# Performance work log

Hardware: AMD Instinct MI355X
Metric: run time of the kernel (lower is better)

Reference implementation:

```python
import jax, jax.numpy as jnp
import numpy as np

N = 16384
DIM_IN = 128
DIM_OUT = 128
HIDDEN = (DIM_IN + DIM_OUT) // 2  # 128


def setup_inputs() -> dict:
    key = jax.random.key(0)
    ks = jax.random.split(key, 8)
    s_in = 1.0 / np.sqrt(DIM_IN)
    s_h = 1.0 / np.sqrt(HIDDEN)
    return {
        "x": jax.random.normal(ks[0], (N, DIM_IN), dtype=jnp.float32),
        "adj": jax.random.uniform(ks[1], (N, N), dtype=jnp.float32) * (1.0 / N),
        "W2": jax.random.uniform(ks[2], (DIM_IN, HIDDEN), minval=-s_in, maxval=s_in, dtype=jnp.float32),
        "b2": jnp.zeros((HIDDEN,), dtype=jnp.float32),
        "W4": jax.random.uniform(ks[3], (HIDDEN, DIM_OUT), minval=-s_h, maxval=s_h, dtype=jnp.float32),
        "b4": jnp.zeros((DIM_OUT,), dtype=jnp.float32),
        "res_w": jax.random.uniform(ks[4], (DIM_OUT, HIDDEN), minval=-s_h, maxval=s_h, dtype=jnp.float32),
        "res_b": jax.random.uniform(ks[5], (DIM_OUT,), minval=-s_h, maxval=s_h, dtype=jnp.float32),
    }


def gcn(x, adj, W, b):
    # GraphConvolution: support = x @ W; out = adj @ support + b
    return adj @ (x @ W) + b


def reference(x, adj, W2, b2, W4, b4, res_w, res_b):
    local_hidden = gcn(x, adj, W2, b2)          # [N, HIDDEN]
    local_cross = gcn(local_hidden, adj, W4, b4)  # [N, DIM_OUT]
    # addRes: residual linear projection of local_hidden
    embed = local_cross + local_hidden @ res_w.T + res_b
    return embed
```

## Files before the change

kernel.cpp:

```cpp
#include <hip/hip_runtime.h>
#include <hip/hip_bf16.h>

#define MN 16384
#define SPLITS 4
#define KSLICE (MN / SPLITS)
#define BK 64
#define NSTEPS (KSLICE / BK)

typedef float f32x4 __attribute__((ext_vector_type(4)));
typedef int   i32x4 __attribute__((ext_vector_type(4)));

#define A8S 32768.0f
#define SB1 64.0f
#define SB2 4096.0f
#define SC1 (1.0f / (32768.0f * 64.0f))
#define SC2 (1.0f / (32768.0f * 4096.0f))

__device__ __forceinline__ void async16(void* lds, const void* g) {
  __builtin_amdgcn_global_load_lds(
      (const __attribute__((address_space(1))) unsigned int*)g,
      (__attribute__((address_space(3))) unsigned int*)lds, 16, 0, 0);
}


__global__ __launch_bounds__(256)
void k1_xw2(const float* __restrict__ x, const float* __restrict__ W2,
            unsigned char* __restrict__ B1) {
  __shared__ __align__(16) float xs[64 * 128];
  const int t = threadIdx.x;
  const long rowbase = (long)blockIdx.x * 64;
  const f32x4* xg = (const f32x4*)(x + rowbase * 128);
  f32x4* xl = (f32x4*)xs;
#pragma unroll
  for (int i = 0; i < 8; ++i) xl[t + 256 * i] = xg[t + 256 * i];
  __syncthreads();
  const int r0 = (t >> 5) * 8;
  const int c0 = (t & 31) * 4;
  float acc[8][4] = {};
  for (int k = 0; k < 128; k += 4) {
    f32x4 w[4];
#pragma unroll
    for (int kk = 0; kk < 4; ++kk) w[kk] = *(const f32x4*)(W2 + (k + kk) * 128 + c0);
#pragma unroll
    for (int i = 0; i < 8; ++i) {
      f32x4 xv = *(const f32x4*)(xs + (r0 + i) * 128 + k);
#pragma unroll
      for (int kk = 0; kk < 4; ++kk)
#pragma unroll
        for (int j = 0; j < 4; ++j) acc[i][j] += xv[kk] * w[kk][j];
    }
  }
  const long U = (rowbase + r0) >> 3;
  i32x4 wv0, wv1;
#pragma unroll
  for (int j = 0; j < 4; ++j) {
    int lo = __builtin_amdgcn_cvt_pk_fp8_f32(acc[0][j] * SB1, acc[1][j] * SB1, 0, false);
    lo     = __builtin_amdgcn_cvt_pk_fp8_f32(acc[2][j] * SB1, acc[3][j] * SB1, lo, true);
    int hi = __builtin_amdgcn_cvt_pk_fp8_f32(acc[4][j] * SB1, acc[5][j] * SB1, 0, false);
    hi     = __builtin_amdgcn_cvt_pk_fp8_f32(acc[6][j] * SB1, acc[7][j] * SB1, hi, true);
    if (j < 2) { wv0[2 * j] = lo; wv0[2 * j + 1] = hi; }
    else       { wv1[2 * (j - 2)] = lo; wv1[2 * (j - 2) + 1] = hi; }
  }
  *(i32x4*)(B1 + (U * 128 + c0) * 8)      = wv0;
  *(i32x4*)(B1 + (U * 128 + c0) * 8 + 16) = wv1;
}

template <int AMODE>
__global__ __launch_bounds__(256, 4)
void big_mm(const float* __restrict__ A, const unsigned char* __restrict__ A8r,
            unsigned char* __restrict__ A8w, const unsigned char* __restrict__ B8,
            float sc, float* __restrict__ P) {
  __shared__ __align__(16) unsigned char Bs[3 * 8192];
  const int tid  = threadIdx.x;
  const int wid  = tid >> 6;
  const int lane = tid & 63;
  const int g    = lane >> 4;
  const int cl   = lane & 15;
  const int tile_m = blockIdx.x & 255;
  const int s      = blockIdx.x >> 8;
  const long k0 = (long)s * KSLICE;

  const char* bsrc = (const char*)B8 + k0 * 128 + (long)tid * 16;
  const float* aptr = nullptr;
  if constexpr (AMODE != 1)
    aptr = A + (long)(tile_m * 64 + wid * 16 + cl) * MN + k0 + 16 * g;
  const long c8base = (long)blockIdx.x * (64L * 4096) + (long)tid * 16;

  f32x4 acc[8] = {};

  {
    unsigned char* d0 = Bs + wid * 1024;
    async16(d0, bsrc);          async16(d0 + 4096, bsrc + 4096);
    unsigned char* d1 = Bs + 8192 + wid * 1024;
    async16(d1, bsrc + 8192);   async16(d1 + 4096, bsrc + 12288);
  }
  f32x4 a0n, a1n, a2n, a3n;
  i32x4 q8n;
  if constexpr (AMODE == 1) {
    q8n = *(const i32x4*)(A8r + c8base);
  } else {
    a0n = *(const f32x4*)aptr;       a1n = *(const f32x4*)(aptr + 4);
    a2n = *(const f32x4*)(aptr + 8); a3n = *(const f32x4*)(aptr + 12);
  }
  __syncthreads();

  int cur = 0, nxt = 2;
  for (int t = 0; t < NSTEPS; ++t) {
    if (t + 2 < NSTEPS) {
      unsigned char* d = Bs + nxt * 8192 + wid * 1024;
      const char* src = bsrc + (long)(t + 2) * 8192;
      async16(d, src);  async16(d + 4096, src + 4096);
    }
    __builtin_amdgcn_sched_barrier(0);

    i32x4 pk;
    if constexpr (AMODE == 1) {
      pk = q8n;
      if (t + 1 < NSTEPS)
        q8n = *(const i32x4*)(A8r + c8base + (long)(t + 1) * 4096);
    } else {
      f32x4 a0 = a0n, a1 = a1n, a2 = a2n, a3 = a3n;
      if (t + 1 < NSTEPS) {
        const float* ap = aptr + (long)(t + 1) * BK;
        a0n = *(const f32x4*)ap;       a1n = *(const f32x4*)(ap + 4);
        a2n = *(const f32x4*)(ap + 8); a3n = *(const f32x4*)(ap + 12);
      }
      pk[0] = __builtin_amdgcn_cvt_pk_fp8_f32(a0[0] * A8S, a0[1] * A8S, 0, false);
      pk[0] = __builtin_amdgcn_cvt_pk_fp8_f32(a0[2] * A8S, a0[3] * A8S, pk[0], true);
      pk[1] = __builtin_amdgcn_cvt_pk_fp8_f32(a1[0] * A8S, a1[1] * A8S, 0, false);
      pk[1] = __builtin_amdgcn_cvt_pk_fp8_f32(a1[2] * A8S, a1[3] * A8S, pk[1], true);
      pk[2] = __builtin_amdgcn_cvt_pk_fp8_f32(a2[0] * A8S, a2[1] * A8S, 0, false);
      pk[2] = __builtin_amdgcn_cvt_pk_fp8_f32(a2[2] * A8S, a2[3] * A8S, pk[2], true);
      pk[3] = __builtin_amdgcn_cvt_pk_fp8_f32(a3[0] * A8S, a3[1] * A8S, 0, false);
      pk[3] = __builtin_amdgcn_cvt_pk_fp8_f32(a3[2] * A8S, a3[3] * A8S, pk[3], true);
      if constexpr (AMODE == 0)
        __builtin_nontemporal_store(pk, (i32x4*)(A8w + c8base + (long)t * 4096));
    }
    const long alo = ((long)(unsigned)pk[1] << 32) | (unsigned)pk[0];
    const long ahi = ((long)(unsigned)pk[3] << 32) | (unsigned)pk[2];

    const char* bb = (const char*)Bs + cur * 8192 + g * 2048 + cl * 8;
#pragma unroll
    for (int c = 0; c < 8; ++c) {
      long b0 = *(const long*)(bb + c * 128);
      long b1 = *(const long*)(bb + 1024 + c * 128);
      acc[c] = __builtin_amdgcn_mfma_f32_16x16x32_fp8_fp8(alo, b0, acc[c], 0, 0, 0);
      acc[c] = __builtin_amdgcn_mfma_f32_16x16x32_fp8_fp8(ahi, b1, acc[c], 0, 0, 0);
    }

    if (t < NSTEPS - 2) {
      if constexpr (AMODE == 0)      asm volatile("s_waitcnt vmcnt(7)" ::: "memory");
      else if constexpr (AMODE == 2) asm volatile("s_waitcnt vmcnt(6)" ::: "memory");
      else                           asm volatile("s_waitcnt vmcnt(3)" ::: "memory");
    } else {
      asm volatile("s_waitcnt vmcnt(0)" ::: "memory");
    }
    __builtin_amdgcn_s_barrier();
    cur = (cur == 2) ? 0 : cur + 1;
    nxt = (nxt == 2) ? 0 : nxt + 1;
  }

  float* pb = P + ((long)s * MN + tile_m * 64 + wid * 16) * 128;
#pragma unroll
  for (int c = 0; c < 8; ++c)
#pragma unroll
    for (int q = 0; q < 4; ++q)
      __builtin_nontemporal_store(acc[c][q] * sc,
                                  &pb[(g * 4 + q) * 128 + 16 * c + cl]);
}

__global__ __launch_bounds__(256)
void k3_mid(const float* __restrict__ P, const float* __restrict__ b2,
            const float* __restrict__ W4, const float* __restrict__ res_w,
            const float* __restrict__ b4, const float* __restrict__ res_b,
            unsigned char* __restrict__ B2, float* __restrict__ Rr) {
  __shared__ __align__(16) float hs[64 * 128];
  const int t = threadIdx.x;
  const long rowbase = (long)blockIdx.x * 64;
  const long base = rowbase * 32;
  const f32x4* P0 = (const f32x4*)P + base;
  const f32x4* P1 = (const f32x4*)P + (long)MN * 32 + base;
  const f32x4* P2 = (const f32x4*)P + 2L * MN * 32 + base;
  const f32x4* P3 = (const f32x4*)P + 3L * MN * 32 + base;
  const f32x4* b2v = (const f32x4*)b2;
  f32x4* hl = (f32x4*)hs;
#pragma unroll
  for (int i = 0; i < 8; ++i) {
    int idx = t + 256 * i;
    f32x4 v = __builtin_nontemporal_load(P0 + idx);
    v += __builtin_nontemporal_load(P1 + idx);
    v += __builtin_nontemporal_load(P2 + idx);
    v += __builtin_nontemporal_load(P3 + idx);
    hl[idx] = v + b2v[idx & 31];
  }
  __syncthreads();
  const int r0 = (t >> 5) * 8;
  const int c0 = (t & 31) * 4;
  float acc2[8][4] = {};
  float accR[8][4] = {};
  for (int k = 0; k < 128; k += 4) {
    f32x4 w4v[4], rwv[4];
#pragma unroll
    for (int kk = 0; kk < 4; ++kk) w4v[kk] = *(const f32x4*)(W4 + (k + kk) * 128 + c0);
#pragma unroll
    for (int j = 0; j < 4; ++j) rwv[j] = *(const f32x4*)(res_w + (c0 + j) * 128 + k);
#pragma unroll
    for (int i = 0; i < 8; ++i) {
      f32x4 xv = *(const f32x4*)(hs + (r0 + i) * 128 + k);
#pragma unroll
      for (int kk = 0; kk < 4; ++kk)
#pragma unroll
        for (int j = 0; j < 4; ++j) {
          acc2[i][j] += xv[kk] * w4v[kk][j];
          accR[i][j] += xv[kk] * rwv[j][kk];
        }
    }
  }
  const long U = (rowbase + r0) >> 3;
  i32x4 wv0, wv1;
#pragma unroll
  for (int j = 0; j < 4; ++j) {
    int lo = __builtin_amdgcn_cvt_pk_fp8_f32(acc2[0][j] * SB2, acc2[1][j] * SB2, 0, false);
    lo     = __builtin_amdgcn_cvt_pk_fp8_f32(acc2[2][j] * SB2, acc2[3][j] * SB2, lo, true);
    int hi = __builtin_amdgcn_cvt_pk_fp8_f32(acc2[4][j] * SB2, acc2[5][j] * SB2, 0, false);
    hi     = __builtin_amdgcn_cvt_pk_fp8_f32(acc2[6][j] * SB2, acc2[7][j] * SB2, hi, true);
    if (j < 2) { wv0[2 * j] = lo; wv0[2 * j + 1] = hi; }
    else       { wv1[2 * (j - 2)] = lo; wv1[2 * (j - 2) + 1] = hi; }
  }
  *(i32x4*)(B2 + (U * 128 + c0) * 8)      = wv0;
  *(i32x4*)(B2 + (U * 128 + c0) * 8 + 16) = wv1;

  const f32x4 b4v = *(const f32x4*)(b4 + c0);
  const f32x4 rbv = *(const f32x4*)(res_b + c0);
#pragma unroll
  for (int i = 0; i < 8; ++i) {
    f32x4 rv;
#pragma unroll
    for (int j = 0; j < 4; ++j) rv[j] = accR[i][j];
    rv += b4v + rbv;
    *(f32x4*)(Rr + (rowbase + r0 + i) * 128 + c0) = rv;
  }
}

__global__ __launch_bounds__(256)
void k5_out(const float* __restrict__ P, const float* __restrict__ Rr,
            float* __restrict__ out) {
  const long i = (long)blockIdx.x * 256 + threadIdx.x;
  const f32x4* P0 = (const f32x4*)P;
  const f32x4* P1 = P0 + (long)MN * 32;
  const f32x4* P2 = P0 + 2L * MN * 32;
  const f32x4* P3 = P0 + 3L * MN * 32;
  f32x4 v = __builtin_nontemporal_load(P0 + i);
  v += __builtin_nontemporal_load(P1 + i);
  v += __builtin_nontemporal_load(P2 + i);
  v += __builtin_nontemporal_load(P3 + i);
  v += *((const f32x4*)Rr + i);
  __builtin_nontemporal_store(v, (f32x4*)out + i);
}

extern "C" void kernel_launch(void* const* d_in, const int* in_sizes, int n_in,
                              void* d_out, int out_size, void* d_ws, size_t ws_size,
                              hipStream_t stream) {
  const float* x     = (const float*)d_in[0];
  const float* adj   = (const float*)d_in[1];
  const float* W2    = (const float*)d_in[2];
  const float* b2    = (const float*)d_in[3];
  const float* W4    = (const float*)d_in[4];
  const float* b4    = (const float*)d_in[5];
  const float* res_w = (const float*)d_in[6];
  const float* res_b = (const float*)d_in[7];
  float* out = (float*)d_out;

  char* ws = (char*)d_ws;
  unsigned char* B1 = (unsigned char*)ws;
  unsigned char* B2 = (unsigned char*)(ws + (4L << 20));
  float* Rr = (float*)(ws + (8L << 20));
  float* P  = (float*)(ws + (16L << 20));
  unsigned char* A8 = (unsigned char*)(ws + (48L << 20));

  const size_t need = (48L << 20) + (size_t)MN * MN;
  const bool fp8_copy = ws_size >= need;

  k1_xw2<<<dim3(256), dim3(256), 0, stream>>>(x, W2, B1);
  if (fp8_copy) {
    big_mm<0><<<dim3(256 * SPLITS), dim3(256), 0, stream>>>(adj, nullptr, A8, B1, SC1, P);
    k3_mid<<<dim3(256), dim3(256), 0, stream>>>(P, b2, W4, res_w, b4, res_b, B2, Rr);
    big_mm<1><<<dim3(256 * SPLITS), dim3(256), 0, stream>>>(nullptr, A8, nullptr, B2, SC2, P);
  } else {
    big_mm<2><<<dim3(256 * SPLITS), dim3(256), 0, stream>>>(adj, nullptr, nullptr, B1, SC1, P);
    k3_mid<<<dim3(256), dim3(256), 0, stream>>>(P, b2, W4, res_w, b4, res_b, B2, Rr);
    big_mm<2><<<dim3(256 * SPLITS), dim3(256), 0, stream>>>(adj, nullptr, nullptr, B2, SC2, P);
  }
  k5_out<<<dim3(2048), dim3(256), 0, stream>>>(P, Rr, out);
}
```

Measured before the change: 443.5 us.

## Double K-step and rows per block, switch to double-buffered B staging

```diff
diff --git a/kernel.cpp b/kernel.cpp
--- a/kernel.cpp
+++ b/kernel.cpp
@@ -4,7 +4,7 @@
 #define MN 16384
 #define SPLITS 4
 #define KSLICE (MN / SPLITS)
-#define BK 64
+#define BK 128
 #define NSTEPS (KSLICE / BK)
 
 typedef float f32x4 __attribute__((ext_vector_type(4)));
@@ -66,101 +66,97 @@
 }
 
 template <int AMODE>
-__global__ __launch_bounds__(256, 4)
+__global__ __launch_bounds__(512, 4)
 void big_mm(const float* __restrict__ A, const unsigned char* __restrict__ A8r,
             unsigned char* __restrict__ A8w, const unsigned char* __restrict__ B8,
             float sc, float* __restrict__ P) {
-  __shared__ __align__(16) unsigned char Bs[3 * 8192];
+  __shared__ __align__(16) unsigned char Bs[2][16384];
   const int tid  = threadIdx.x;
   const int wid  = tid >> 6;
   const int lane = tid & 63;
   const int g    = lane >> 4;
   const int cl   = lane & 15;
-  const int tile_m = blockIdx.x & 255;
-  const int s      = blockIdx.x >> 8;
+  const int tile_m = blockIdx.x & 127;
+  const int s      = blockIdx.x >> 7;
   const long k0 = (long)s * KSLICE;
 
   const char* bsrc = (const char*)B8 + k0 * 128 + (long)tid * 16;
   const float* aptr = nullptr;
   if constexpr (AMODE != 1)
-    aptr = A + (long)(tile_m * 64 + wid * 16 + cl) * MN + k0 + 16 * g;
-  const long c8base = (long)blockIdx.x * (64L * 4096) + (long)tid * 16;
+    aptr = A + (long)(tile_m * 128 + wid * 16 + cl) * MN + k0 + 32 * g;
+  const long c8base = (long)blockIdx.x * (NSTEPS * 16384L) + (long)tid * 32;
 
   f32x4 acc[8] = {};
 
   {
-    unsigned char* d0 = Bs + wid * 1024;
-    async16(d0, bsrc);          async16(d0 + 4096, bsrc + 4096);
-    unsigned char* d1 = Bs + 8192 + wid * 1024;
-    async16(d1, bsrc + 8192);   async16(d1 + 4096, bsrc + 12288);
-  }
-  f32x4 a0n, a1n, a2n, a3n;
-  i32x4 q8n;
+    unsigned char* d = &Bs[0][0] + wid * 1024;
+    async16(d, bsrc);
+    async16(d + 8192, bsrc + 8192);
+  }
+  i32x4 av0, av1;
   if constexpr (AMODE == 1) {
-    q8n = *(const i32x4*)(A8r + c8base);
-  } else {
-    a0n = *(const f32x4*)aptr;       a1n = *(const f32x4*)(aptr + 4);
-    a2n = *(const f32x4*)(aptr + 8); a3n = *(const f32x4*)(aptr + 12);
+    av0 = *(const i32x4*)(A8r + c8base);
+    av1 = *(const i32x4*)(A8r + c8base + 16);
   }
   __syncthreads();
 
-  int cur = 0, nxt = 2;
-  for (int t = 0; t < NSTEPS; ++t) {
-    if (t + 2 < NSTEPS) {
-      unsigned char* d = Bs + nxt * 8192 + wid * 1024;
-      const char* src = bsrc + (long)(t + 2) * 8192;
-      async16(d, src);  async16(d + 4096, src + 4096);
+  for (int T = 0; T < NSTEPS; ++T) {
+    if (T + 1 < NSTEPS) {
+      unsigned char* d = &Bs[(T + 1) & 1][0] + wid * 1024;
+      const char* src = bsrc + (long)(T + 1) * 16384;
+      async16(d, src);
+      async16(d + 8192, src + 8192);
     }
     __builtin_amdgcn_sched_barrier(0);
 
-    i32x4 pk;
+    int pk[8];
+    i32x4 nav0, nav1;
     if constexpr (AMODE == 1) {
-      pk = q8n;
-      if (t + 1 < NSTEPS)
-        q8n = *(const i32x4*)(A8r + c8base + (long)(t + 1) * 4096);
+      if (T + 1 < NSTEPS) {
+        const unsigned char* ap = A8r + c8base + (long)(T + 1) * 16384;
+        nav0 = *(const i32x4*)ap;
+        nav1 = *(const i32x4*)(ap + 16);
+      }
+      pk[0] = av0[0]; pk[1] = av0[1]; pk[2] = av0[2]; pk[3] = av0[3];
+      pk[4] = av1[0]; pk[5] = av1[1]; pk[6] = av1[2]; pk[7] = av1[3];
     } else {
-      f32x4 a0 = a0n, a1 = a1n, a2 = a2n, a3 = a3n;
-      if (t + 1 < NSTEPS) {
-        const float* ap = aptr + (long)(t + 1) * BK;
-        a0n = *(const f32x4*)ap;       a1n = *(const f32x4*)(ap + 4);
-        a2n = *(const f32x4*)(ap + 8); a3n = *(const f32x4*)(ap + 12);
-      }
-      pk[0] = __builtin_amdgcn_cvt_pk_fp8_f32(a0[0] * A8S, a0[1] * A8S, 0, false);
-      pk[0] = __builtin_amdgcn_cvt_pk_fp8_f32(a0[2] * A8S, a0[3] * A8S, pk[0], true);
-      pk[1] = __builtin_amdgcn_cvt_pk_fp8_f32(a1[0] * A8S, a1[1] * A8S, 0, false);
-      pk[1] = __builtin_amdgcn_cvt_pk_fp8_f32(a1[2] * A8S, a1[3] * A8S, pk[1], true);
-      pk[2] = __builtin_amdgcn_cvt_pk_fp8_f32(a2[0] * A8S, a2[1] * A8S, 0, false);
-      pk[2] = __builtin_amdgcn_cvt_pk_fp8_f32(a2[2] * A8S, a2[3] * A8S, pk[2], true);
-      pk[3] = __builtin_amdgcn_cvt_pk_fp8_f32(a3[0] * A8S, a3[1] * A8S, 0, false);
-      pk[3] = __builtin_amdgcn_cvt_pk_fp8_f32(a3[2] * A8S, a3[3] * A8S, pk[3], true);
-      if constexpr (AMODE == 0)
-        __builtin_nontemporal_store(pk, (i32x4*)(A8w + c8base + (long)t * 4096));
-    }
-    const long alo = ((long)(unsigned)pk[1] << 32) | (unsigned)pk[0];
-    const long ahi = ((long)(unsigned)pk[3] << 32) | (unsigned)pk[2];
-
-    const char* bb = (const char*)Bs + cur * 8192 + g * 2048 + cl * 8;
-#pragma unroll
-    for (int c = 0; c < 8; ++c) {
-      long b0 = *(const long*)(bb + c * 128);
-      long b1 = *(const long*)(bb + 1024 + c * 128);
-      acc[c] = __builtin_amdgcn_mfma_f32_16x16x32_fp8_fp8(alo, b0, acc[c], 0, 0, 0);
-      acc[c] = __builtin_amdgcn_mfma_f32_16x16x32_fp8_fp8(ahi, b1, acc[c], 0, 0, 0);
-    }
-
-    if (t < NSTEPS - 2) {
-      if constexpr (AMODE == 0)      asm volatile("s_waitcnt vmcnt(7)" ::: "memory");
-      else if constexpr (AMODE == 2) asm volatile("s_waitcnt vmcnt(6)" ::: "memory");
-      else                           asm volatile("s_waitcnt vmcnt(3)" ::: "memory");
-    } else {
-      asm volatile("s_waitcnt vmcnt(0)" ::: "memory");
+      const float* ap = aptr + (long)T * BK;
+      f32x4 av[8];
+#pragma unroll
+      for (int i = 0; i < 8; ++i) av[i] = *(const f32x4*)(ap + 4 * i);
+#pragma unroll
+      for (int d = 0; d < 8; ++d) {
+        int w = __builtin_amdgcn_cvt_pk_fp8_f32(av[d][0] * A8S, av[d][1] * A8S, 0, false);
+        pk[d] = __builtin_amdgcn_cvt_pk_fp8_f32(av[d][2] * A8S, av[d][3] * A8S, w, true);
+      }
+      if constexpr (AMODE == 0) {
+        i32x4 s1 = {pk[0], pk[1], pk[2], pk[3]};
+        i32x4 s2 = {pk[4], pk[5], pk[6], pk[7]};
+        unsigned char* wp = A8w + c8base + (long)T * 16384;
+        __builtin_nontemporal_store(s1, (i32x4*)wp);
+        __builtin_nontemporal_store(s2, (i32x4*)(wp + 16));
+      }
+    }
+
+    const char* bb = (const char*)&Bs[T & 1][0] + g * 4096 + cl * 8;
+#pragma unroll
+    for (int j = 0; j < 4; ++j) {
+      const long a = ((long)(unsigned)pk[2 * j + 1] << 32) | (unsigned)pk[2 * j];
+#pragma unroll
+      for (int c = 0; c < 8; ++c) {
+        long b = *(const long*)(bb + j * 1024 + c * 128);
+        acc[c] = __builtin_amdgcn_mfma_f32_16x16x32_fp8_fp8(a, b, acc[c], 0, 0, 0);
+      }
+    }
+
+    if constexpr (AMODE == 1) {
+      if (T + 1 < NSTEPS) asm volatile("s_waitcnt vmcnt(2)" ::: "memory");
+      av0 = nav0; av1 = nav1;
     }
     __builtin_amdgcn_s_barrier();
-    cur = (cur == 2) ? 0 : cur + 1;
-    nxt = (nxt == 2) ? 0 : nxt + 1;
-  }
-
-  float* pb = P + ((long)s * MN + tile_m * 64 + wid * 16) * 128;
+  }
+
+  float* pb = P + ((long)s * MN + tile_m * 128 + wid * 16) * 128;
 #pragma unroll
   for (int c = 0; c < 8; ++c)
 #pragma unroll
@@ -283,13 +279,13 @@
 
   k1_xw2<<<dim3(256), dim3(256), 0, stream>>>(x, W2, B1);
   if (fp8_copy) {
-    big_mm<0><<<dim3(256 * SPLITS), dim3(256), 0, stream>>>(adj, nullptr, A8, B1, SC1, P);
+    big_mm<0><<<dim3(128 * SPLITS), dim3(512), 0, stream>>>(adj, nullptr, A8, B1, SC1, P);
     k3_mid<<<dim3(256), dim3(256), 0, stream>>>(P, b2, W4, res_w, b4, res_b, B2, Rr);
-    big_mm<1><<<dim3(256 * SPLITS), dim3(256), 0, stream>>>(nullptr, A8, nullptr, B2, SC2, P);
+    big_mm<1><<<dim3(128 * SPLITS), dim3(512), 0, stream>>>(nullptr, A8, nullptr, B2, SC2, P);
   } else {
-    big_mm<2><<<dim3(256 * SPLITS), dim3(256), 0, stream>>>(adj, nullptr, nullptr, B1, SC1, P);
+    big_mm<2><<<dim3(128 * SPLITS), dim3(512), 0, stream>>>(adj, nullptr, nullptr, B1, SC1, P);
     k3_mid<<<dim3(256), dim3(256), 0, stream>>>(P, b2, W4, res_w, b4, res_b, B2, Rr);
-    big_mm<2><<<dim3(256 * SPLITS), dim3(256), 0, stream>>>(adj, nullptr, nullptr, B2, SC2, P);
+    big_mm<2><<<dim3(128 * SPLITS), dim3(512), 0, stream>>>(adj, nullptr, nullptr, B2, SC2, P);
   }
   k5_out<<<dim3(2048), dim3(256), 0, stream>>>(P, Rr, out);
 }
```

New measurement: 595.0 us. 34.2% more time.

## Double-buffer B tiles in two-step supersteps to halve barriers in big_mm

Applied to the files above, without the earlier changes.

```diff
diff --git a/kernel.cpp b/kernel.cpp
--- a/kernel.cpp
+++ b/kernel.cpp
@@ -6,6 +6,7 @@
 #define KSLICE (MN / SPLITS)
 #define BK 64
 #define NSTEPS (KSLICE / BK)
+#define NSUPER (NSTEPS / 2)
 
 typedef float f32x4 __attribute__((ext_vector_type(4)));
 typedef int   i32x4 __attribute__((ext_vector_type(4)));
@@ -70,7 +71,7 @@
 void big_mm(const float* __restrict__ A, const unsigned char* __restrict__ A8r,
             unsigned char* __restrict__ A8w, const unsigned char* __restrict__ B8,
             float sc, float* __restrict__ P) {
-  __shared__ __align__(16) unsigned char Bs[3 * 8192];
+  __shared__ __align__(16) unsigned char Bs[2][16384];
   const int tid  = threadIdx.x;
   const int wid  = tid >> 6;
   const int lane = tid & 63;
@@ -89,10 +90,9 @@
   f32x4 acc[8] = {};
 
   {
-    unsigned char* d0 = Bs + wid * 1024;
-    async16(d0, bsrc);          async16(d0 + 4096, bsrc + 4096);
-    unsigned char* d1 = Bs + 8192 + wid * 1024;
-    async16(d1, bsrc + 8192);   async16(d1 + 4096, bsrc + 12288);
+    unsigned char* d = &Bs[0][0] + wid * 1024;
+    async16(d, bsrc);                 async16(d + 4096, bsrc + 4096);
+    async16(d + 8192, bsrc + 8192);   async16(d + 12288, bsrc + 12288);
   }
   f32x4 a0n, a1n, a2n, a3n;
   i32x4 q8n;
@@ -104,60 +104,63 @@
   }
   __syncthreads();
 
-  int cur = 0, nxt = 2;
-  for (int t = 0; t < NSTEPS; ++t) {
-    if (t + 2 < NSTEPS) {
-      unsigned char* d = Bs + nxt * 8192 + wid * 1024;
-      const char* src = bsrc + (long)(t + 2) * 8192;
-      async16(d, src);  async16(d + 4096, src + 4096);
+  for (int m = 0; m < NSUPER; ++m) {
+    if (m + 1 < NSUPER) {
+      unsigned char* d = &Bs[(m + 1) & 1][0] + wid * 1024;
+      const char* src = bsrc + (long)(2 * m + 2) * 8192;
+      async16(d, src);                 async16(d + 4096, src + 4096);
+      async16(d + 8192, src + 8192);   async16(d + 12288, src + 12288);
     }
     __builtin_amdgcn_sched_barrier(0);
 
-    i32x4 pk;
-    if constexpr (AMODE == 1) {
-      pk = q8n;
-      if (t + 1 < NSTEPS)
-        q8n = *(const i32x4*)(A8r + c8base + (long)(t + 1) * 4096);
-    } else {
-      f32x4 a0 = a0n, a1 = a1n, a2 = a2n, a3 = a3n;
-      if (t + 1 < NSTEPS) {
-        const float* ap = aptr + (long)(t + 1) * BK;
-        a0n = *(const f32x4*)ap;       a1n = *(const f32x4*)(ap + 4);
-        a2n = *(const f32x4*)(ap + 8); a3n = *(const f32x4*)(ap + 12);
+#pragma unroll
+    for (int h = 0; h < 2; ++h) {
+      const int t = 2 * m + h;
+      int pk0, pk1, pk2, pk3;
+      if constexpr (AMODE == 1) {
+        i32x4 q8 = q8n;
+        if (t + 1 < NSTEPS)
+          q8n = *(const i32x4*)(A8r + c8base + (long)(t + 1) * 4096);
+        pk0 = q8[0]; pk1 = q8[1]; pk2 = q8[2]; pk3 = q8[3];
+      } else {
+        f32x4 a0 = a0n, a1 = a1n, a2 = a2n, a3 = a3n;
+        if (t + 1 < NSTEPS) {
+          const float* ap = aptr + (long)(t + 1) * BK;
+          a0n = *(const f32x4*)ap;       a1n = *(const f32x4*)(ap + 4);
+          a2n = *(const f32x4*)(ap + 8); a3n = *(const f32x4*)(ap + 12);
+        }
+        pk0 = __builtin_amdgcn_cvt_pk_fp8_f32(a0[0] * A8S, a0[1] * A8S, 0, false);
+        pk0 = __builtin_amdgcn_cvt_pk_fp8_f32(a0[2] * A8S, a0[3] * A8S, pk0, true);
+        pk1 = __builtin_amdgcn_cvt_pk_fp8_f32(a1[0] * A8S, a1[1] * A8S, 0, false);
+        pk1 = __builtin_amdgcn_cvt_pk_fp8_f32(a1[2] * A8S, a1[3] * A8S, pk1, true);
+        pk2 = __builtin_amdgcn_cvt_pk_fp8_f32(a2[0] * A8S, a2[1] * A8S, 0, false);
+        pk2 = __builtin_amdgcn_cvt_pk_fp8_f32(a2[2] * A8S, a2[3] * A8S, pk2, true);
+        pk3 = __builtin_amdgcn_cvt_pk_fp8_f32(a3[0] * A8S, a3[1] * A8S, 0, false);
+        pk3 = __builtin_amdgcn_cvt_pk_fp8_f32(a3[2] * A8S, a3[3] * A8S, pk3, true);
+        if constexpr (AMODE == 0) {
+          i32x4 st = {pk0, pk1, pk2, pk3};
+          __builtin_nontemporal_store(st, (i32x4*)(A8w + c8base + (long)t * 4096));
+        }
       }
-      pk[0] = __builtin_amdgcn_cvt_pk_fp8_f32(a0[0] * A8S, a0[1] * A8S, 0, false);
-      pk[0] = __builtin_amdgcn_cvt_pk_fp8_f32(a0[2] * A8S, a0[3] * A8S, pk[0], true);
-      pk[1] = __builtin_amdgcn_cvt_pk_fp8_f32(a1[0] * A8S, a1[1] * A8S, 0, false);
-      pk[1] = __builtin_amdgcn_cvt_pk_fp8_f32(a1[2] * A8S, a1[3] * A8S, pk[1], true);
-      pk[2] = __builtin_amdgcn_cvt_pk_fp8_f32(a2[0] * A8S, a2[1] * A8S, 0, false);
-      pk[2] = __builtin_amdgcn_cvt_pk_fp8_f32(a2[2] * A8S, a2[3] * A8S, pk[2], true);
-      pk[3] = __builtin_amdgcn_cvt_pk_fp8_f32(a3[0] * A8S, a3[1] * A8S, 0, false);
-      pk[3] = __builtin_amdgcn_cvt_pk_fp8_f32(a3[2] * A8S, a3[3] * A8S, pk[3], true);
-      if constexpr (AMODE == 0)
-        __builtin_nontemporal_store(pk, (i32x4*)(A8w + c8base + (long)t * 4096));
-    }
-    const long alo = ((long)(unsigned)pk[1] << 32) | (unsigned)pk[0];
-    const long ahi = ((long)(unsigned)pk[3] << 32) | (unsigned)pk[2];
-
-    const char* bb = (const char*)Bs + cur * 8192 + g * 2048 + cl * 8;
-#pragma unroll
-    for (int c = 0; c < 8; ++c) {
-      long b0 = *(const long*)(bb + c * 128);
-      long b1 = *(const long*)(bb + 1024 + c * 128);
-      acc[c] = __builtin_amdgcn_mfma_f32_16x16x32_fp8_fp8(alo, b0, acc[c], 0, 0, 0);
-      acc[c] = __builtin_amdgcn_mfma_f32_16x16x32_fp8_fp8(ahi, b1, acc[c], 0, 0, 0);
-    }
-
-    if (t < NSTEPS - 2) {
-      if constexpr (AMODE == 0)      asm volatile("s_waitcnt vmcnt(7)" ::: "memory");
-      else if constexpr (AMODE == 2) asm volatile("s_waitcnt vmcnt(6)" ::: "memory");
-      else                           asm volatile("s_waitcnt vmcnt(3)" ::: "memory");
-    } else {
-      asm volatile("s_waitcnt vmcnt(0)" ::: "memory");
-    }
-    __builtin_amdgcn_s_barrier();
-    cur = (cur == 2) ? 0 : cur + 1;
-    nxt = (nxt == 2) ? 0 : nxt + 1;
+      const long alo = ((long)(unsigned)pk1 << 32) | (unsigned)pk0;
+      const long ahi = ((long)(unsigned)pk3 << 32) | (unsigned)pk2;
+
+      const char* bb = (const char*)&Bs[m & 1][0] + h * 8192 + g * 2048 + cl * 8;
+#pragma unroll
+      for (int c = 0; c < 8; ++c) {
+        long b0 = *(const long*)(bb + c * 128);
+        long b1 = *(const long*)(bb + 1024 + c * 128);
+        acc[c] = __builtin_amdgcn_mfma_f32_16x16x32_fp8_fp8(alo, b0, acc[c], 0, 0, 0);
+        acc[c] = __builtin_amdgcn_mfma_f32_16x16x32_fp8_fp8(ahi, b1, acc[c], 0, 0, 0);
+      }
+    }
+
+    if (m + 1 < NSUPER) {
+      if constexpr (AMODE == 0)      asm volatile("s_waitcnt vmcnt(10)" ::: "memory");
+      else if constexpr (AMODE == 2) asm volatile("s_waitcnt vmcnt(8)" ::: "memory");
+      else                           asm volatile("s_waitcnt vmcnt(2)" ::: "memory");
+      __builtin_amdgcn_s_barrier();
+    }
   }
 
   float* pb = P + ((long)s * MN + tile_m * 64 + wid * 16) * 128;
```

Result: faster. 429.9 us (-3.1%).
